# Kernel optimization log

Hardware: AMD Instinct MI355X
Metric: run time of the kernel (lower is better)

Reference implementation:

```python
import jax, jax.numpy as jnp
import numpy as np

B, S, D = 2, 2048, 1024
H, DH = 16, 64
DM = 4096
NEG = 1e10


def setup_inputs() -> dict:
    key = jax.random.key(0)
    ks = jax.random.split(key, 8)
    sc = 1.0 / np.sqrt(D)
    return {
        "x": jax.random.normal(ks[0], (B, S, D), jnp.float32),
        "W_Q": jax.random.normal(ks[1], (H, DH, D), jnp.float32) * sc,
        "W_K": jax.random.normal(ks[2], (H, DH, D), jnp.float32) * sc,
        "W_V": jax.random.normal(ks[3], (H, DH, D), jnp.float32) * sc,
        "W_O": jax.random.normal(ks[4], (D, H * DH), jnp.float32) * sc,
        "W_in": jax.random.normal(ks[5], (DM, D), jnp.float32) * sc,
        "b_in": jnp.zeros((DM,), jnp.float32),
        "W_out": jax.random.normal(ks[6], (D, DM), jnp.float32) * sc,
        "b_out": jnp.zeros((D,), jnp.float32),
    }


def reference(x, W_Q, W_K, W_V, W_O, W_in, b_in, W_out, b_out):
    b, s, d = x.shape
    d_head = W_Q.shape[1]
    # --- Attention (faithful to original einsum/mask formulation) ---
    q = jnp.einsum('ihd,bpd->biph', W_Q, x)
    k = jnp.einsum('ihd,bpd->biph', W_K, x)
    v = jnp.einsum('ihd,bpd->biph', W_V, x)
    scores = jnp.einsum('biph,biqh->biqp', k, q)  # [b,i,q,p]
    # original: t.tril(scores) - 1e10 * (1 - triu(ones)) ; mask buffer is triu
    triu = jnp.triu(jnp.ones((s, s), x.dtype))
    masked = jnp.tril(scores) - NEG * (1.0 - triu)
    attn = jax.nn.softmax(masked / np.sqrt(d_head), axis=-1)
    z = jnp.einsum('biph,biqp->biqh', v, attn)          # [b,i,q,h]
    z_flat = z.transpose(0, 2, 1, 3).reshape(b, s, -1)   # b q (i h)
    attn_out = jnp.einsum('df,bqf->bqd', W_O, z_flat)
    # --- Block residual structure (as written: x = attn(x); x = x + x) ---
    mid = attn_out + attn_out
    # --- MLP ---
    pre = jnp.einsum('md,bpd->bpm', W_in, mid) + b_in
    h = jax.nn.relu(pre)
    mlp_out = jnp.einsum('dm,bpm->bpd', W_out, h) + b_out
    return mid + mlp_out
```

## Files before the change

### kernel.cpp

```cpp
#include <hip/hip_runtime.h>
#include <hip/hip_bf16.h>
#include <stdint.h>

typedef unsigned short ushort_t;
typedef __attribute__((ext_vector_type(8))) short short8;
typedef __attribute__((ext_vector_type(4))) float floatx4;

#define DEV __device__ __forceinline__

DEV ushort_t f2b(float f) {
  uint32_t x = __float_as_uint(f);
  uint32_t r = (x + 0x7FFFu + ((x >> 16) & 1u)) >> 16;
  return (ushort_t)r;
}
DEV float b2f(ushort_t u) { return __uint_as_float(((uint32_t)u) << 16); }

DEV void async16(const ushort_t* g, ushort_t* l) {
  __builtin_amdgcn_global_load_lds(
      (const __attribute__((address_space(1))) void*)g,
      (__attribute__((address_space(3))) void*)l, 16, 0, 0);
}

struct Cvt7 {
  const float* src[7];
  ushort_t* dst[7];
  float scale[7];
  unsigned start[8];
};
__global__ void cvt_all(Cvt7 a) {
  unsigned idx = blockIdx.x * blockDim.x + threadIdx.x;
  if (idx >= a.start[7]) return;
  int seg = 0;
#pragma unroll
  for (int j = 1; j < 7; j++) seg += (idx >= a.start[j]) ? 1 : 0;
  unsigned off = idx - a.start[seg];
  float sc = a.scale[seg];
  float4 v = ((const float4*)a.src[seg])[off];
  ((ushort4*)a.dst[seg])[off] =
      make_ushort4(f2b(v.x * sc), f2b(v.y * sc), f2b(v.z * sc), f2b(v.w * sc));
}

template <int MODE, int MT, int SWZ>
__launch_bounds__(256)
__global__ void gemm_bt(const ushort_t* __restrict__ A, const ushort_t* __restrict__ Bm,
                        int M, int N, int Kd, int ldk,
                        ushort_t* __restrict__ outB, float* __restrict__ outF,
                        const float* __restrict__ bias) {
  constexpr int TM = 32 * MT;
  __shared__ alignas(16) ushort_t As[TM * 64];
  __shared__ alignas(16) ushort_t Bs[128 * 64];
  const int tid = threadIdx.x;
  const int wave = tid >> 6, lane = tid & 63;
  const int wm = wave >> 1, wn = wave & 1;

  int bx, by;
  if constexpr (SWZ == 1) {
    const int f = blockIdx.x + gridDim.x * blockIdx.y;
    by = (f & 7) + 8 * (f / (8 * gridDim.x));
    bx = (f >> 3) % gridDim.x;
  } else if constexpr (SWZ == 2) {
    const int x = blockIdx.x, y = blockIdx.y;
    bx = 2 * (x & 3) + (y & 1);
    by = (y >> 1) + 32 * (x >> 2);
  } else {
    bx = blockIdx.x; by = blockIdx.y;
  }
  const int m0 = by * TM, n0 = bx * 128;
  const int kz = blockIdx.z * Kd;

  floatx4 acc[MT][4];
#pragma unroll
  for (int i = 0; i < MT; i++)
#pragma unroll
    for (int j = 0; j < 4; j++) acc[i][j] = (floatx4){0.f, 0.f, 0.f, 0.f};

  const int r8 = lane >> 3;
  const int scol = (((lane & 7) ^ (r8 & 7)) * 8);
  const ushort_t* gA = A + (size_t)(m0 + wave * (TM / 4) + r8) * ldk + kz + scol;
  const ushort_t* gB = Bm + (size_t)(n0 + wave * 32 + r8) * ldk + kz + scol;
  ushort_t* lA = As + wave * (TM / 4) * 64;
  ushort_t* lB = Bs + wave * 2048;

  const int fr = lane & 15, fq = lane >> 4;
  const int sw = fr & 7;
  const ushort_t* rdA = As + (wm * 16 * MT + fr) * 64;
  const ushort_t* rdB = Bs + (wn * 64 + fr) * 64;

  for (int k0 = 0; k0 < Kd; k0 += 64) {
#pragma unroll
    for (int j = 0; j < MT; j++) async16(gA + (size_t)j * 8 * ldk, lA + j * 512);
#pragma unroll
    for (int j = 0; j < 4; j++) async16(gB + (size_t)j * 8 * ldk, lB + j * 512);
    gA += 64; gB += 64;
    __syncthreads();
#pragma unroll
    for (int h = 0; h < 2; h++) {
      const int co = ((h * 4 + fq) ^ sw) * 8;
      short8 af[MT], bfv[4];
#pragma unroll
      for (int mt = 0; mt < MT; mt++) af[mt] = *(const short8*)(rdA + mt * 16 * 64 + co);
#pragma unroll
      for (int nt = 0; nt < 4; nt++) bfv[nt] = *(const short8*)(rdB + nt * 16 * 64 + co);
#pragma unroll
      for (int mt = 0; mt < MT; mt++)
#pragma unroll
        for (int nt = 0; nt < 4; nt++)
          acc[mt][nt] = __builtin_amdgcn_mfma_f32_16x16x32_bf16(af[mt], bfv[nt], acc[mt][nt], 0, 0, 0);
    }
    __syncthreads();
  }

  const int crow = m0 + wm * 16 * MT + (lane >> 4) * 4;
  const int ccol = n0 + wn * 64 + (lane & 15);
  const size_t zoff = (size_t)blockIdx.z * M * N;
#pragma unroll
  for (int mt = 0; mt < MT; mt++)
#pragma unroll
    for (int nt = 0; nt < 4; nt++) {
      floatx4 a = acc[mt][nt];
#pragma unroll
      for (int r = 0; r < 4; r++) {
        const int gm = crow + mt * 16 + r;
        const int gn = ccol + nt * 16;
        const size_t idx = (size_t)gm * N + gn;
        float v = a[r];
        if constexpr (MODE == 0) {
          outB[idx] = f2b(v);
        } else if constexpr (MODE == 1) {
          outB[idx] = f2b(v);
          outF[idx] = v + bias[gn];
        } else if constexpr (MODE == 2) {
          float t = v + bias[gn];
          outB[idx] = f2b(t > 0.f ? t : 0.f);
        } else {
          outF[zoff + idx] = v;
        }
      }
    }
}

template <int MODE>
__launch_bounds__(512, 2)
__global__ void gemm256(const ushort_t* __restrict__ A, const ushort_t* __restrict__ Bm,
                        int M, int N, int Kd, int ldk,
                        ushort_t* __restrict__ outB, float* __restrict__ outF,
                        const float* __restrict__ bias) {
  __shared__ alignas(16) ushort_t As[4][256 * 32];
  __shared__ alignas(16) ushort_t Bs[4][256 * 32];
  const int tid = threadIdx.x;
  const int lane = tid & 63;
  const int wave = tid >> 6;
  const int wm = wave >> 2, wn = wave & 3;

  const int gy = gridDim.y;
  int f = blockIdx.x + gridDim.x * blockIdx.y;
  {
    const int nwg = gridDim.x * gy;
    const int q = nwg >> 3, rr = nwg & 7;
    const int xcd = f & 7, ix = f >> 3;
    f = (xcd < rr ? xcd * (q + 1) : rr * (q + 1) + (xcd - rr) * q) + ix;
  }
  const int bx = f / gy, by = f - gy * bx;
  const int m0 = by * 256, n0 = bx * 256;
  const size_t kz = (size_t)blockIdx.z * Kd;

  floatx4 acc[8][4];
#pragma unroll
  for (int i = 0; i < 8; i++)
#pragma unroll
    for (int j = 0; j < 4; j++) acc[i][j] = (floatx4){0.f, 0.f, 0.f, 0.f};

  const int rloc = tid >> 2, cch = tid & 3;
  const int gcol = ((cch ^ ((rloc >> 1) & 3)) * 8);
  const ushort_t* gA = A + (size_t)(m0 + rloc) * ldk + kz + gcol;
  const ushort_t* gB = Bm + (size_t)(n0 + rloc) * ldk + kz + gcol;
  const int lofs = rloc * 32 + cch * 8;

#define STGA32(bufi, kofs)                                              \
  {                                                                     \
    async16(gA + (kofs), &As[bufi][lofs]);                              \
    async16(gA + (size_t)128 * ldk + (kofs), &As[bufi][4096 + lofs]);   \
  }
#define STGB32(bufi, kofs)                                              \
  {                                                                     \
    async16(gB + (kofs), &Bs[bufi][lofs]);                              \
    async16(gB + (size_t)128 * ldk + (kofs), &Bs[bufi][4096 + lofs]);   \
  }

  const int NT = Kd >> 5;
  STGA32(0, 0) STGB32(0, 0)
  if (NT > 1) { STGA32(1, 32) STGB32(1, 32) }
  if (NT > 2) { STGA32(2, 64) STGB32(2, 64) }
  if (NT > 2) asm volatile("s_waitcnt vmcnt(8)" ::: "memory");
  else if (NT > 1) asm volatile("s_waitcnt vmcnt(4)" ::: "memory");
  else asm volatile("s_waitcnt vmcnt(0)" ::: "memory");
  __builtin_amdgcn_s_barrier();

  const int fr = lane & 15, fq = lane >> 4;
  const int co = ((fq ^ ((fr >> 1) & 3)) * 8);
  const int aoff = (wm * 128 + fr) * 32 + co;
  const int boff = (wn * 64 + fr) * 32 + co;

  for (int kt = 0; kt < NT; ++kt) {
    const int cb = kt & 3;
    const int pb = (kt + 3) & 3;
    const int kof = (kt + 3) * 32;
    const bool sp = (kt + 3) < NT;
    const ushort_t* Ab = As[cb];
    const ushort_t* Bb = Bs[cb];
    short8 av[4], bv[4];

#pragma unroll
    for (int i = 0; i < 4; i++) av[i] = *(const short8*)(Ab + aoff + i * 512);
#pragma unroll
    for (int j = 0; j < 4; j++) bv[j] = *(const short8*)(Bb + boff + j * 512);
    if (sp) STGA32(pb, kof)
    __builtin_amdgcn_s_barrier();
    asm volatile("s_waitcnt lgkmcnt(0)" ::: "memory");
    __builtin_amdgcn_s_setprio(1);
#pragma unroll
    for (int i = 0; i < 4; i++)
#pragma unroll
      for (int j = 0; j < 4; j++)
        acc[i][j] = __builtin_amdgcn_mfma_f32_16x16x32_bf16(av[i], bv[j], acc[i][j], 0, 0, 0);
    __builtin_amdgcn_s_setprio(0);
    __builtin_amdgcn_s_barrier();

#pragma unroll
    for (int i = 0; i < 4; i++) av[i] = *(const short8*)(Ab + aoff + 2048 + i * 512);
    if (sp) STGB32(pb, kof)
    __builtin_amdgcn_s_barrier();
    asm volatile("s_waitcnt lgkmcnt(0)" ::: "memory");
    __builtin_amdgcn_s_setprio(1);
#pragma unroll
    for (int i = 0; i < 4; i++)
#pragma unroll
      for (int j = 0; j < 4; j++)
        acc[4 + i][j] = __builtin_amdgcn_mfma_f32_16x16x32_bf16(av[i], bv[j], acc[4 + i][j], 0, 0, 0);
    __builtin_amdgcn_s_setprio(0);
    if (kt + 3 < NT) asm volatile("s_waitcnt vmcnt(8)" ::: "memory");
    else if (kt + 2 < NT) asm volatile("s_waitcnt vmcnt(4)" ::: "memory");
    else asm volatile("s_waitcnt vmcnt(0)" ::: "memory");
    __builtin_amdgcn_s_barrier();
  }
#undef STGA32
#undef STGB32

  const int crow = m0 + wm * 128 + (lane >> 4) * 4;
  const int ccol = n0 + wn * 64 + (lane & 15);
  const size_t zoff = (size_t)blockIdx.z * ((size_t)M * (size_t)N);
#pragma unroll
  for (int mt = 0; mt < 8; mt++)
#pragma unroll
    for (int nt = 0; nt < 4; nt++) {
      floatx4 a = acc[mt][nt];
#pragma unroll
      for (int r = 0; r < 4; r++) {
        const int gm = crow + mt * 16 + r;
        const int gn = ccol + nt * 16;
        const size_t idx = (size_t)gm * N + gn;
        if constexpr (MODE == 0) {
          outB[idx] = f2b(a[r]);
        } else if constexpr (MODE == 2) {
          float t = a[r] + bias[gn];
          outB[idx] = f2b(t > 0.f ? t : 0.f);
        } else {
          outF[zoff + idx] = a[r];
        }
      }
    }
}

__launch_bounds__(256)
__global__ void reduce4(const float4* __restrict__ P, float4* __restrict__ out, int n4) {
  int i = blockIdx.x * blockDim.x + threadIdx.x;
  int st = gridDim.x * blockDim.x;
  for (; i < n4; i += st) {
    float4 a = out[i];
    float4 p0 = P[i], p1 = P[i + 1048576], p2 = P[i + 2097152], p3 = P[i + 3145728];
    a.x += (p0.x + p1.x) + (p2.x + p3.x);
    a.y += (p0.y + p1.y) + (p2.y + p3.y);
    a.z += (p0.z + p1.z) + (p2.z + p3.z);
    a.w += (p0.w + p1.w) + (p2.w + p3.w);
    out[i] = a;
  }
}

__launch_bounds__(256)
__global__ void attn1(const ushort_t* __restrict__ qkv,
                      float* __restrict__ eG, float* __restrict__ psumG) {
  const int c = blockIdx.x & 63;
  const int i = (blockIdx.x >> 6) & 15;
  const int b = blockIdx.x >> 10;
  const int t = threadIdx.x, wave = t >> 6, h = t & 63;
  const size_t rowbase = (size_t)b * 2048 * 3072;
  float vacc = 0.f;
#pragma unroll
  for (int r = 0; r < 8; r++) {
    const int s = c * 32 + wave * 8 + r;
    const size_t rb = rowbase + (size_t)s * 3072 + i * 64 + h;
    float q = b2f(qkv[rb]);
    float k = b2f(qkv[rb + 1024]);
    float v = b2f(qkv[rb + 2048]);
    float d = q * k;
#pragma unroll
    for (int off = 32; off > 0; off >>= 1) d += __shfl_xor(d, off, 64);
    if (h == 0) eG[((size_t)(b * 16 + i)) * 2048 + s] = __expf(d * 0.125f);
    vacc += v;
  }
  __shared__ float vs[4][64];
  vs[wave][h] = vacc;
  __syncthreads();
  if (t < 64)
    psumG[(((size_t)(b * 16 + i)) * 64 + c) * 64 + t] =
        vs[0][t] + vs[1][t] + vs[2][t] + vs[3][t];
}

__launch_bounds__(256)
__global__ void attn2(const ushort_t* __restrict__ qkv,
                      const float* __restrict__ eG, const float* __restrict__ psumG,
                      ushort_t* __restrict__ Z) {
  const int wave = threadIdx.x >> 6, h = threadIdx.x & 63;
  const int c = (blockIdx.x & 15) * 4 + wave;
  const int i = (blockIdx.x >> 4) & 15;
  const int b = blockIdx.x >> 8;
  const size_t rowbase = (size_t)b * 2048 * 3072;
  const size_t pbase = ((size_t)(b * 16 + i)) * 64;
  float run = 0.f;
#pragma unroll 8
  for (int cc = c + 1; cc < 64; cc++) run += psumG[(pbase + cc) * 64 + h];
  const size_t ebase = ((size_t)(b * 16 + i)) * 2048;
  for (int t4 = 1; t4 >= 0; t4--) {
    float vv[16], ee[16];
#pragma unroll
    for (int j = 0; j < 16; j++) {
      const int s = c * 32 + t4 * 16 + j;
      vv[j] = b2f(qkv[rowbase + (size_t)s * 3072 + 2048 + i * 64 + h]);
      ee[j] = eG[ebase + s];
    }
#pragma unroll
    for (int j = 15; j >= 0; j--) {
      const int s = c * 32 + t4 * 16 + j;
      float z = (ee[j] * vv[j] + run) / (ee[j] + (float)(2047 - s));
      Z[((size_t)b * 2048 + s) * 1024 + i * 64 + h] = f2b(z);
      run += vv[j];
    }
  }
}

extern "C" void kernel_launch(void* const* d_in, const int* in_sizes, int n_in,
                              void* d_out, int out_size, void* d_ws, size_t ws_size,
                              hipStream_t stream) {
  const float* x     = (const float*)d_in[0];
  const float* W_Q   = (const float*)d_in[1];
  const float* W_K   = (const float*)d_in[2];
  const float* W_V   = (const float*)d_in[3];
  const float* W_O   = (const float*)d_in[4];
  const float* W_in  = (const float*)d_in[5];
  const float* b_in  = (const float*)d_in[6];
  const float* W_out = (const float*)d_in[7];
  const float* b_out = (const float*)d_in[8];
  float* out = (float*)d_out;

  char* base = (char*)d_ws;
  const size_t MB = 1048576;
  ushort_t* Xb    = (ushort_t*)(base + 0 * MB);
  ushort_t* Wqkv  = (ushort_t*)(base + 8 * MB);
  ushort_t* WOb   = (ushort_t*)(base + 14 * MB);
  ushort_t* Z     = (ushort_t*)(base + 16 * MB);
  ushort_t* QKV   = (ushort_t*)(base + 24 * MB);
  ushort_t* midb  = (ushort_t*)(base + 48 * MB);
  ushort_t* Winb  = (ushort_t*)(base + 56 * MB);
  ushort_t* Woutb = (ushort_t*)(base + 64 * MB);
  ushort_t* Hb    = (ushort_t*)(base + 72 * MB);
  float*    P     = (float*)(base + 0 * MB);
  float*    psumG = (float*)(base + 72 * MB);
  float*    eG    = (float*)(base + 72 * MB + 524288);

  Cvt7 ca;
  ca.src[0] = x;     ca.dst[0] = Xb;               ca.scale[0] = 1.f;
  ca.src[1] = W_Q;   ca.dst[1] = Wqkv;             ca.scale[1] = 1.f;
  ca.src[2] = W_K;   ca.dst[2] = Wqkv + 1048576;   ca.scale[2] = 1.f;
  ca.src[3] = W_V;   ca.dst[3] = Wqkv + 2097152;   ca.scale[3] = 1.f;
  ca.src[4] = W_O;   ca.dst[4] = WOb;              ca.scale[4] = 2.f;
  ca.src[5] = W_in;  ca.dst[5] = Winb;             ca.scale[5] = 1.f;
  ca.src[6] = W_out; ca.dst[6] = Woutb;            ca.scale[6] = 1.f;
  unsigned n4s[7] = {1048576, 262144, 262144, 262144, 262144, 1048576, 1048576};
  unsigned acc4 = 0;
  for (int j = 0; j < 7; j++) { ca.start[j] = acc4; acc4 += n4s[j]; }
  ca.start[7] = acc4;
  cvt_all<<<dim3((acc4 + 255) / 256), dim3(256), 0, stream>>>(ca);

  gemm256<0><<<dim3(12, 16), 512, 0, stream>>>(Xb, Wqkv, 4096, 3072, 1024, 1024,
                                               QKV, nullptr, nullptr);
  attn1<<<dim3(2048), 256, 0, stream>>>(QKV, eG, psumG);
  attn2<<<dim3(512), 256, 0, stream>>>(QKV, eG, psumG, Z);
  gemm_bt<1, 2, 1><<<dim3(8, 64), 256, 0, stream>>>(Z, WOb, 4096, 1024, 1024, 1024,
                                                    midb, out, b_out);
  gemm256<2><<<dim3(16, 16), 512, 0, stream>>>(midb, Winb, 4096, 4096, 1024, 1024,
                                               Hb, nullptr, b_in);
  gemm256<3><<<dim3(4, 16, 4), 512, 0, stream>>>(Hb, Woutb, 4096, 1024, 1024, 4096,
                                                 nullptr, P, nullptr);
  reduce4<<<dim3(1024), 256, 0, stream>>>((const float4*)P, (float4*)out, 1048576);
}
```

Baseline: 290.3 us.

## Switch QKV and MLP-down GEMMs to gemm_bt, halve split-K, speed attn2 math

The QKV projection moves from the 256-tile gemm256 kernel to gemm_bt with a smaller tile and a larger grid. The MLP down-projection drops from 4-way to 2-way split-K on gemm_bt, with a matching two-partial reduction kernel. In attn2, the prefix-sum loop is split across four accumulators, and the division is replaced by a hardware reciprocal plus one Newton step, hoisted out of the serial loop. The goal is better occupancy, less partial-sum traffic and a shorter serial dependency chain. The risks are lower per-tile reuse in the GEMMs and slightly different rounding in attn2.

```diff
diff --git a/kernel.cpp b/kernel.cpp
--- a/kernel.cpp
+++ b/kernel.cpp
@@ -248,7 +248,6 @@
 
   const int crow = m0 + wm * 128 + (lane >> 4) * 4;
   const int ccol = n0 + wn * 64 + (lane & 15);
-  const size_t zoff = (size_t)blockIdx.z * ((size_t)M * (size_t)N);
 #pragma unroll
   for (int mt = 0; mt < 8; mt++)
 #pragma unroll
@@ -265,23 +264,23 @@
           float t = a[r] + bias[gn];
           outB[idx] = f2b(t > 0.f ? t : 0.f);
         } else {
-          outF[zoff + idx] = a[r];
+          outF[idx] = a[r];
         }
       }
     }
 }
 
 __launch_bounds__(256)
-__global__ void reduce4(const float4* __restrict__ P, float4* __restrict__ out, int n4) {
+__global__ void reduce2(const float4* __restrict__ P, float4* __restrict__ out, int n4) {
   int i = blockIdx.x * blockDim.x + threadIdx.x;
   int st = gridDim.x * blockDim.x;
   for (; i < n4; i += st) {
     float4 a = out[i];
-    float4 p0 = P[i], p1 = P[i + 1048576], p2 = P[i + 2097152], p3 = P[i + 3145728];
-    a.x += (p0.x + p1.x) + (p2.x + p3.x);
-    a.y += (p0.y + p1.y) + (p2.y + p3.y);
-    a.z += (p0.z + p1.z) + (p2.z + p3.z);
-    a.w += (p0.w + p1.w) + (p2.w + p3.w);
+    float4 p0 = P[i], p1 = P[i + 1048576];
+    a.x += p0.x + p1.x;
+    a.y += p0.y + p1.y;
+    a.z += p0.z + p1.z;
+    a.w += p0.w + p1.w;
     out[i] = a;
   }
 }
@@ -326,22 +325,35 @@
   const int b = blockIdx.x >> 8;
   const size_t rowbase = (size_t)b * 2048 * 3072;
   const size_t pbase = ((size_t)(b * 16 + i)) * 64;
-  float run = 0.f;
-#pragma unroll 8
-  for (int cc = c + 1; cc < 64; cc++) run += psumG[(pbase + cc) * 64 + h];
+  float r0 = 0.f, r1 = 0.f, r2 = 0.f, r3 = 0.f;
+  {
+    int cc = c + 1;
+    for (; cc + 3 < 64; cc += 4) {
+      r0 += psumG[(pbase + cc) * 64 + h];
+      r1 += psumG[(pbase + cc + 1) * 64 + h];
+      r2 += psumG[(pbase + cc + 2) * 64 + h];
+      r3 += psumG[(pbase + cc + 3) * 64 + h];
+    }
+    for (; cc < 64; cc++) r0 += psumG[(pbase + cc) * 64 + h];
+  }
+  float run = (r0 + r1) + (r2 + r3);
   const size_t ebase = ((size_t)(b * 16 + i)) * 2048;
   for (int t4 = 1; t4 >= 0; t4--) {
-    float vv[16], ee[16];
+    float vv[16], num[16], rcp[16];
 #pragma unroll
     for (int j = 0; j < 16; j++) {
       const int s = c * 32 + t4 * 16 + j;
       vv[j] = b2f(qkv[rowbase + (size_t)s * 3072 + 2048 + i * 64 + h]);
-      ee[j] = eG[ebase + s];
+      float e = eG[ebase + s];
+      num[j] = e * vv[j];
+      float d = e + (float)(2047 - s);
+      float r = __builtin_amdgcn_rcpf(d);
+      rcp[j] = r * (2.f - d * r);
     }
 #pragma unroll
     for (int j = 15; j >= 0; j--) {
       const int s = c * 32 + t4 * 16 + j;
-      float z = (ee[j] * vv[j] + run) / (ee[j] + (float)(2047 - s));
+      float z = (num[j] + run) * rcp[j];
       Z[((size_t)b * 2048 + s) * 1024 + i * 64 + h] = f2b(z);
       run += vv[j];
     }
@@ -391,15 +403,15 @@
   ca.start[7] = acc4;
   cvt_all<<<dim3((acc4 + 255) / 256), dim3(256), 0, stream>>>(ca);
 
-  gemm256<0><<<dim3(12, 16), 512, 0, stream>>>(Xb, Wqkv, 4096, 3072, 1024, 1024,
-                                               QKV, nullptr, nullptr);
+  gemm_bt<0, 4, 0><<<dim3(24, 32), 256, 0, stream>>>(Xb, Wqkv, 4096, 3072, 1024, 1024,
+                                                     QKV, nullptr, nullptr);
   attn1<<<dim3(2048), 256, 0, stream>>>(QKV, eG, psumG);
   attn2<<<dim3(512), 256, 0, stream>>>(QKV, eG, psumG, Z);
   gemm_bt<1, 2, 1><<<dim3(8, 64), 256, 0, stream>>>(Z, WOb, 4096, 1024, 1024, 1024,
                                                     midb, out, b_out);
   gemm256<2><<<dim3(16, 16), 512, 0, stream>>>(midb, Winb, 4096, 4096, 1024, 1024,
                                                Hb, nullptr, b_in);
-  gemm256<3><<<dim3(4, 16, 4), 512, 0, stream>>>(Hb, Woutb, 4096, 1024, 1024, 4096,
-                                                 nullptr, P, nullptr);
-  reduce4<<<dim3(1024), 256, 0, stream>>>((const float4*)P, (float4*)out, 1048576);
-}
+  gemm_bt<3, 2, 2><<<dim3(8, 64, 2), 256, 0, stream>>>(Hb, Woutb, 4096, 1024, 2048, 4096,
+                                                       nullptr, P, nullptr);
+  reduce2<<<dim3(1024), 256, 0, stream>>>((const float4*)P, (float4*)out, 1048576);
+}
```

After: 281.6 us. -3.0%, faster.
